# Kernel optimization log

Measured on AMD Instinct MI355X. Metric: run time of the kernel, lower is better.

Reference implementation:

```python
import jax, jax.numpy as jnp
import numpy as np

BATCH, SEQ, E, H = 8, 2048, 1024, 1024
LEAK = 0.95
SPECTRAL_RADIUS = 1.2
SPARSITY = 0.1


def setup_inputs() -> dict:
    rng = np.random.default_rng(0)
    x = rng.standard_normal((BATCH, SEQ, E)).astype(np.float32)
    # W_in: kaiming_uniform-like init
    bound = np.sqrt(1.0 / E)
    W_in = rng.uniform(-bound, bound, (H, E)).astype(np.float32)
    # W_res: sparse normal, rescaled to spectral radius 1.2
    W_res = rng.standard_normal((H, H)).astype(np.float32)
    mask = (rng.random((H, H)) > SPARSITY).astype(np.float32)
    W_res *= mask
    rad = np.max(np.abs(np.linalg.eigvals(W_res.astype(np.float64))))
    W_res = (W_res * (SPECTRAL_RADIUS / (rad + 1e-8))).astype(np.float32)
    s = 0.02
    inp = {
        "x": jnp.asarray(x),
        "W_in": jnp.asarray(W_in),
        "W_res": jnp.asarray(W_res),
        "norm_g": jnp.ones((E,), jnp.float32),
        "norm_b": jnp.zeros((E,), jnp.float32),
        "delta_w": jnp.asarray(rng.standard_normal((1, E)).astype(np.float32) * s),
        "delta_b": jnp.zeros((1,), jnp.float32),
        "A": jnp.full((H,), -10.0, jnp.float32),
        "B_w": jnp.asarray(rng.standard_normal((H, E)).astype(np.float32) * s),
        "ro_g": jnp.ones((H,), jnp.float32),
        "ro_b": jnp.zeros((H,), jnp.float32),
        "ro_w": jnp.asarray(rng.standard_normal((E, H)).astype(np.float32) * s),
        "ro_bias": jnp.zeros((E,), jnp.float32),
        "gate_w": jnp.asarray(rng.standard_normal((E, E)).astype(np.float32) * s),
        "gate_b": jnp.zeros((E,), jnp.float32),
    }
    return inp


def _layernorm(x, g, b, eps=1e-5):
    m = jnp.mean(x, axis=-1, keepdims=True)
    v = jnp.mean((x - m) ** 2, axis=-1, keepdims=True)
    return (x - m) * jax.lax.rsqrt(v + eps) * g + b


def reference(x, W_in, W_res, norm_g, norm_b, delta_w, delta_b, A, B_w,
              ro_g, ro_b, ro_w, ro_bias, gate_w, gate_b):
    x_norm = _layernorm(x, norm_g, norm_b)                      # [B,S,E]

    # --- TrueReservoir: leaky tanh RNN (scan over seq) ---
    xin = jnp.einsum('bse,he->bsh', x_norm, W_in)               # [B,S,H]
    h0 = jnp.zeros((x.shape[0], W_res.shape[0]), x.dtype)

    def res_step(h, u):
        new = jnp.tanh(u + h @ W_res.T)
        new = LEAK * new + (1.0 - LEAK) * h
        return new, new

    _, res_states = jax.lax.scan(res_step, h0, jnp.swapaxes(xin, 0, 1))
    res_states = jnp.swapaxes(res_states, 0, 1)                 # [B,S,H]

    ro_in = _layernorm(res_states, ro_g, ro_b)
    reservoir_out = jax.nn.gelu(jnp.einsum('bsh,eh->bse', ro_in, ro_w) + ro_bias,
                                approximate=False)              # [B,S,E]

    # --- selective SSM-style scan ---
    Bx = jnp.einsum('bse,he->bsh', x_norm, B_w)                 # [B,S,H]
    delta = jax.nn.softplus(jnp.einsum('bse,oe->bso', x_norm, delta_w) + delta_b)  # [B,S,1]
    A_bar = jnp.exp(A * delta)                                  # [B,S,H]
    B_bar = Bx * (1.0 - A_bar) / (A + 1e-8)                     # [B,S,H]

    def ssm_step(h, ab):
        a, b = ab
        h = a * h + b
        return h, h

    _, ssm_states = jax.lax.scan(
        ssm_step, h0, (jnp.swapaxes(A_bar, 0, 1), jnp.swapaxes(B_bar, 0, 1)))
    ssm_states = jnp.swapaxes(ssm_states, 0, 1)                 # [B,S,H]

    gate = jax.nn.sigmoid(jnp.einsum('bse,fe->bsf', x, gate_w) + gate_b)  # [B,S,E]
    return reservoir_out * gate + ssm_states * (1.0 - gate)
```

## Files before the change

### kernel.cpp

```cpp
#include <hip/hip_runtime.h>
#include <math.h>

#define B_ 8
#define S_ 2048
#define E_ 1024
#define H_ 1024
#define M_ 16384

typedef __attribute__((ext_vector_type(8))) short short8;
typedef __attribute__((ext_vector_type(4))) float floatx4;

__device__ __forceinline__ void block_reduce2(float &a, float &b) {
#pragma unroll
  for (int off = 32; off > 0; off >>= 1) {
    a += __shfl_down(a, off);
    b += __shfl_down(b, off);
  }
  __shared__ float sa[4], sb[4];
  const int w = threadIdx.x >> 6;
  __syncthreads();
  if ((threadIdx.x & 63) == 0) { sa[w] = a; sb[w] = b; }
  __syncthreads();
  a = sa[0] + sa[1] + sa[2] + sa[3];
  b = sb[0] + sb[1] + sb[2] + sb[3];
}

__device__ __forceinline__ unsigned pack_bf16(float lo, float hi) {
  return __builtin_amdgcn_perm(__float_as_uint(hi) + 0x8000u,
                               __float_as_uint(lo) + 0x8000u, 0x07060302u);
}
__device__ __forceinline__ unsigned pack_hi16(unsigned a, unsigned b) {
  return __builtin_amdgcn_perm(b, a, 0x07060302u);
}

__global__ __launch_bounds__(256) void ln_delta_kernel(
    const float* __restrict__ x, const float* __restrict__ g, const float* __restrict__ bt,
    const float* __restrict__ dw, const float* __restrict__ db,
    unsigned short* __restrict__ xnb, float* __restrict__ delta)
{
  const int row = blockIdx.x;
  const int t = threadIdx.x;
  const float4 v = ((const float4*)(x + (size_t)row * E_))[t];
  float s1 = v.x + v.y + v.z + v.w;
  float s2 = v.x*v.x + v.y*v.y + v.z*v.z + v.w*v.w;
  block_reduce2(s1, s2);
  const float mean = s1 * (1.f / E_);
  const float var  = s2 * (1.f / E_) - mean * mean;
  const float rstd = rsqrtf(var + 1e-5f);
  const float4 g4 = ((const float4*)g)[t];
  const float4 b4 = ((const float4*)bt)[t];
  float4 o;
  o.x = (v.x - mean) * rstd * g4.x + b4.x;
  o.y = (v.y - mean) * rstd * g4.y + b4.y;
  o.z = (v.z - mean) * rstd * g4.z + b4.z;
  o.w = (v.w - mean) * rstd * g4.w + b4.w;
  uint2 p;
  p.x = pack_bf16(o.x, o.y); p.y = pack_bf16(o.z, o.w);
  ((uint2*)(xnb + (size_t)row * E_))[t] = p;
  const float4 d4 = ((const float4*)dw)[t];
  float dd = o.x*d4.x + o.y*d4.y + o.z*d4.z + o.w*d4.w;
  float dummy = 0.f;
  block_reduce2(dd, dummy);
  if (t == 0) {
    const float z = dd + db[0];
    delta[row] = (z > 20.f) ? z : log1pf(__expf(z));
  }
}

__global__ __launch_bounds__(256) void rowstats_kernel(
    const float* __restrict__ res, float2* __restrict__ st)
{
  const int row = blockIdx.x;
  const int t = threadIdx.x;
  const float4 v = ((const float4*)(res + (size_t)row * H_))[t];
  float s1 = v.x + v.y + v.z + v.w;
  float s2 = v.x*v.x + v.y*v.y + v.z*v.z + v.w*v.w;
  block_reduce2(s1, s2);
  if (t == 0) {
    const float m = s1 * (1.f / H_);
    const float var = s2 * (1.f / H_) - m * m;
    st[row] = make_float2(m, rsqrtf(var + 1e-5f));
  }
}

__global__ __launch_bounds__(256) void tobf16_kernel(
    const float* __restrict__ s, unsigned short* __restrict__ d)
{
  const int i = blockIdx.x * 256 + threadIdx.x;
  const float4 v = ((const float4*)s)[i];
  uint2 p;
  p.x = pack_bf16(v.x, v.y); p.y = pack_bf16(v.z, v.w);
  ((uint2*)d)[i] = p;
}

__global__ __launch_bounds__(256) void splitw_kernel(
    const float* __restrict__ s, unsigned short* __restrict__ dh, unsigned short* __restrict__ dl)
{
  const int i = blockIdx.x * 256 + threadIdx.x;
  const float4 v = ((const float4*)s)[i];
  const float sv[4] = {v.x, v.y, v.z, v.w};
  unsigned h[4]; float l[4];
#pragma unroll
  for (int e = 0; e < 4; ++e) {
    h[e] = (__float_as_uint(sv[e]) + 0x8000u) & 0xFFFF0000u;
    l[e] = sv[e] - __uint_as_float(h[e]);
  }
  uint2 ph, pl;
  ph.x = pack_hi16(h[0], h[1]); ph.y = pack_hi16(h[2], h[3]);
  pl.x = pack_bf16(l[0], l[1]); pl.y = pack_bf16(l[2], l[3]);
  ((uint2*)dh)[i] = ph;
  ((uint2*)dl)[i] = pl;
}

__global__ __launch_bounds__(256) void gemm_bb(
    const unsigned short* __restrict__ A, const unsigned short* __restrict__ W,
    float* __restrict__ C)
{
  __shared__ __align__(16) unsigned short As[128 * 40];
  __shared__ __align__(16) unsigned short Ws[128 * 40];
  const int tid  = threadIdx.x;
  const int bn   = blockIdx.x & 7;
  const int bm   = blockIdx.x >> 3;
  const int wave = tid >> 6, lane = tid & 63;
  const int wm = (wave >> 1) * 64, wn = (wave & 1) * 64;
  const int fm = lane & 15, quad = lane >> 4;

  floatx4 acc[4][4];
#pragma unroll
  for (int i = 0; i < 4; ++i)
#pragma unroll
    for (int j = 0; j < 4; ++j) acc[i][j] = (floatx4){0.f, 0.f, 0.f, 0.f};

  const unsigned short* Abase = A + (size_t)bm * 128 * 1024;
  const unsigned short* Wbase = W + (size_t)bn * 128 * 1024;

  for (int k0 = 0; k0 < 1024; k0 += 32) {
    uint2 a2[4], w2[4];
#pragma unroll
    for (int i = 0; i < 4; ++i) {
      const int q = tid + 256 * i;
      const int row = q >> 3, ch = q & 7;
      a2[i] = *(const uint2*)(Abase + (size_t)row * 1024 + k0 + ch * 4);
      w2[i] = *(const uint2*)(Wbase + (size_t)row * 1024 + k0 + ch * 4);
    }
#pragma unroll
    for (int i = 0; i < 4; ++i) {
      const int q = tid + 256 * i;
      const int row = q >> 3, ch = q & 7;
      *(uint2*)(&As[row * 40 + ch * 4]) = a2[i];
      *(uint2*)(&Ws[row * 40 + ch * 4]) = w2[i];
    }
    __syncthreads();
    short8 af[4], wf[4];
#pragma unroll
    for (int i = 0; i < 4; ++i) {
      af[i] = *(const short8*)(&As[(wm + i * 16 + fm) * 40 + quad * 8]);
      wf[i] = *(const short8*)(&Ws[(wn + i * 16 + fm) * 40 + quad * 8]);
    }
#pragma unroll
    for (int i = 0; i < 4; ++i)
#pragma unroll
      for (int j = 0; j < 4; ++j)
        acc[i][j] = __builtin_amdgcn_mfma_f32_16x16x32_bf16(af[i], wf[j], acc[i][j], 0, 0, 0);
    __syncthreads();
  }

#pragma unroll
  for (int i = 0; i < 4; ++i) {
    const int grow0 = bm * 128 + wm + i * 16 + quad * 4;
#pragma unroll
    for (int j = 0; j < 4; ++j) {
      const int gcol = bn * 128 + wn + j * 16 + fm;
#pragma unroll
      for (int r = 0; r < 4; ++r)
        C[(size_t)(grow0 + r) * 1024 + gcol] = acc[i][j][r];
    }
  }
}

__global__ __launch_bounds__(256) void gemm_readout_mfma(
    const float* __restrict__ A,
    const unsigned short* __restrict__ Wh_g,
    const unsigned short* __restrict__ Wl_g,
    const float* __restrict__ bias,
    const float2* __restrict__ lnst,
    const float* __restrict__ lng, const float* __restrict__ lnb,
    const float* __restrict__ Avec,
    const float* __restrict__ cumd,
    const float* __restrict__ chH,
    const float* __restrict__ gate,
    float* __restrict__ C)
{
  __shared__ __align__(16) unsigned short Ah[128 * 40];
  __shared__ __align__(16) unsigned short Al[128 * 40];
  __shared__ __align__(16) unsigned short Wh[128 * 40];
  __shared__ __align__(16) unsigned short Wl[128 * 40];
  const int tid  = threadIdx.x;
  const int bn   = blockIdx.x & 7;
  const int bm   = blockIdx.x >> 3;
  const int wave = tid >> 6, lane = tid & 63;
  const int wm = (wave >> 1) * 64, wn = (wave & 1) * 64;
  const int fm = lane & 15, quad = lane >> 4;

  floatx4 acc[4][4];
#pragma unroll
  for (int i = 0; i < 4; ++i)
#pragma unroll
    for (int j = 0; j < 4; ++j) acc[i][j] = (floatx4){0.f, 0.f, 0.f, 0.f};

  const float* Abase = A + (size_t)bm * 128 * 1024;
  const unsigned short* Whb = Wh_g + (size_t)bn * 128 * 1024;
  const unsigned short* Wlb = Wl_g + (size_t)bn * 128 * 1024;

  float2 st_i[4];
#pragma unroll
  for (int i = 0; i < 4; ++i) {
    const int q = tid + 256 * i;
    st_i[i] = lnst[bm * 128 + (q >> 3)];
  }

  for (int k0 = 0; k0 < 1024; k0 += 32) {
#pragma unroll
    for (int i = 0; i < 4; ++i) {
      const int q = tid + 256 * i;
      const int row = q >> 3, ch = q & 7;
      float4 a4 = *(const float4*)(Abase + (size_t)row * 1024 + k0 + ch * 4);
      const float4 g4 = *(const float4*)(lng + k0 + ch * 4);
      const float4 b4 = *(const float4*)(lnb + k0 + ch * 4);
      const float2 st = st_i[i];
      a4.x = (a4.x - st.x) * st.y * g4.x + b4.x;
      a4.y = (a4.y - st.x) * st.y * g4.y + b4.y;
      a4.z = (a4.z - st.x) * st.y * g4.z + b4.z;
      a4.w = (a4.w - st.x) * st.y * g4.w + b4.w;
      const float av[4] = {a4.x, a4.y, a4.z, a4.w};
      unsigned ah[4]; float alr[4];
#pragma unroll
      for (int e = 0; e < 4; ++e) {
        ah[e] = (__float_as_uint(av[e]) + 0x8000u) & 0xFFFF0000u;
        alr[e] = av[e] - __uint_as_float(ah[e]);
      }
      uint2 pah, pal;
      pah.x = pack_hi16(ah[0], ah[1]); pah.y = pack_hi16(ah[2], ah[3]);
      pal.x = pack_bf16(alr[0], alr[1]); pal.y = pack_bf16(alr[2], alr[3]);
      *(uint2*)(&Ah[row * 40 + ch * 4]) = pah;
      *(uint2*)(&Al[row * 40 + ch * 4]) = pal;
      *(uint2*)(&Wh[row * 40 + ch * 4]) = *(const uint2*)(Whb + (size_t)row * 1024 + k0 + ch * 4);
      *(uint2*)(&Wl[row * 40 + ch * 4]) = *(const uint2*)(Wlb + (size_t)row * 1024 + k0 + ch * 4);
    }
    __syncthreads();
    short8 afh[4], afl[4], wfh[4], wfl[4];
#pragma unroll
    for (int i = 0; i < 4; ++i) {
      const int ao = (wm + i * 16 + fm) * 40 + quad * 8;
      const int wo = (wn + i * 16 + fm) * 40 + quad * 8;
      afh[i] = *(const short8*)(&Ah[ao]);
      afl[i] = *(const short8*)(&Al[ao]);
      wfh[i] = *(const short8*)(&Wh[wo]);
      wfl[i] = *(const short8*)(&Wl[wo]);
    }
#pragma unroll
    for (int i = 0; i < 4; ++i)
#pragma unroll
      for (int j = 0; j < 4; ++j) {
        acc[i][j] = __builtin_amdgcn_mfma_f32_16x16x32_bf16(afh[i], wfh[j], acc[i][j], 0, 0, 0);
        acc[i][j] = __builtin_amdgcn_mfma_f32_16x16x32_bf16(afl[i], wfh[j], acc[i][j], 0, 0, 0);
        acc[i][j] = __builtin_amdgcn_mfma_f32_16x16x32_bf16(afh[i], wfl[j], acc[i][j], 0, 0, 0);
      }
    __syncthreads();
  }

#pragma unroll
  for (int i = 0; i < 4; ++i) {
    const int grow0 = bm * 128 + wm + i * 16 + quad * 4;
    float cd_r[4];
    int hb_r[4];
#pragma unroll
    for (int r = 0; r < 4; ++r) {
      const int gr = grow0 + r;
      const int b = gr >> 11;
      const int c = (gr & 2047) >> 7;
      cd_r[r] = cumd[gr];
      hb_r[r] = (b * 16 + c) << 10;
    }
#pragma unroll
    for (int j = 0; j < 4; ++j) {
      const int gcol = bn * 128 + wn + j * 16 + fm;
      const float Ae = Avec[gcol];
      const float bb = bias[gcol];
#pragma unroll
      for (int r = 0; r < 4; ++r) {
        const int gr = grow0 + r;
        const size_t off = (size_t)gr * 1024 + gcol;
        const float hin = chH[hb_r[r] + gcol];
        const float lcl = C[off];
        const float gt  = gate[off];
        float v = acc[i][j][r] + bb;
        v = 0.5f * v * (1.f + erff(v * 0.70710678118654752f));
        const float p = __expf(Ae * cd_r[r]);
        const float sst = lcl + p * hin;
        C[off] = v * gt + sst * (1.f - gt);
      }
    }
  }
}

__global__ __launch_bounds__(512, 2) void scan_gate_kernel(
    float* __restrict__ xin_res,
    const float* __restrict__ Wres,
    unsigned* __restrict__ hbuf,
    const float* __restrict__ x,
    const float* __restrict__ gate_w,
    const float* __restrict__ gate_b,
    float* __restrict__ gateout,
    const float* __restrict__ delta,
    const float* __restrict__ Avec,
    float* __restrict__ bx,
    float* __restrict__ chP,
    float* __restrict__ cumd)
{
  __shared__ __align__(16) unsigned char smem[20480];
  const int wg  = blockIdx.x;
  const int tid = threadIdx.x;

  if (wg < 128) {
    float* hsb = (float*)smem;
    const int go  = wg & 7;
    const int mem = wg >> 3;
    const int g   = tid >> 6;
    const int l   = tid & 63;
    const int row8 = mem * 64 + g * 8;

    float4 w4[8][4];
#pragma unroll
    for (int r = 0; r < 8; ++r) {
      const float* wrow = Wres + (size_t)(row8 + r) * 1024 + l * 16;
#pragma unroll
      for (int j = 0; j < 4; ++j) w4[r][j] = *(const float4*)(wrow + 4 * j);
    }

    const int m0 = l & 1, m1 = (l >> 1) & 1, m2 = (l >> 2) & 1;
    const int myrow = row8 + (l & 7);
    float hprev = 0.f;
    const unsigned long long tmask = 0x0000FFFF0000FFFFull;

    const int Pw = (tid >> 1) ^ ((tid >> 6) & 7);
    const int wofs = Pw * 4 + (tid & 1) * 2;

    for (int s = 0; s < S_; ++s) {
      const float u = xin_res[((size_t)go * S_ + s) * H_ + myrow];
      asm volatile("" :: "v"(u));

      const unsigned tag = (unsigned)s & 0xFFFFu;
      const unsigned long long tag2 = (unsigned long long)tag | ((unsigned long long)tag << 32);
      const unsigned long long* hp =
          (const unsigned long long*)(hbuf + (size_t)(s & 1) * 8192 + go * 1024) + tid;
      unsigned long long w;
      for (;;) {
        w = __hip_atomic_load(hp, __ATOMIC_RELAXED, __HIP_MEMORY_SCOPE_AGENT);
        if (((w ^ tag2) & tmask) == 0ull) break;
      }

      float2 hf;
      hf.x = __uint_as_float((unsigned)w & 0xFFFF0000u);
      hf.y = __uint_as_float((unsigned)(w >> 32) & 0xFFFF0000u);
      *(float2*)(hsb + (s & 1) * 1024 + wofs) = hf;
      __syncthreads();

      const float* hbse = hsb + (s & 1) * 1024;
      float acc0 = 0.f, acc1 = 0.f, acc2 = 0.f, acc3 = 0.f;
      float acc4 = 0.f, acc5 = 0.f, acc6 = 0.f, acc7 = 0.f;
#pragma unroll
      for (int j = 0; j < 4; ++j) {
        const int P = (4 * l + j) ^ ((l >> 3) & 7);
        const float4 h4 = *(const float4*)(hbse + P * 4);
        acc0 += w4[0][j].x * h4.x + w4[0][j].y * h4.y + w4[0][j].z * h4.z + w4[0][j].w * h4.w;
        acc1 += w4[1][j].x * h4.x + w4[1][j].y * h4.y + w4[1][j].z * h4.z + w4[1][j].w * h4.w;
        acc2 += w4[2][j].x * h4.x + w4[2][j].y * h4.y + w4[2][j].z * h4.z + w4[2][j].w * h4.w;
        acc3 += w4[3][j].x * h4.x + w4[3][j].y * h4.y + w4[3][j].z * h4.z + w4[3][j].w * h4.w;
        acc4 += w4[4][j].x * h4.x + w4[4][j].y * h4.y + w4[4][j].z * h4.z + w4[4][j].w * h4.w;
        acc5 += w4[5][j].x * h4.x + w4[5][j].y * h4.y + w4[5][j].z * h4.z + w4[5][j].w * h4.w;
        acc6 += w4[6][j].x * h4.x + w4[6][j].y * h4.y + w4[6][j].z * h4.z + w4[6][j].w * h4.w;
        acc7 += w4[7][j].x * h4.x + w4[7][j].y * h4.y + w4[7][j].z * h4.z + w4[7][j].w * h4.w;
      }

      float v0 = (m0 ? acc1 : acc0) + __shfl_xor(m0 ? acc0 : acc1, 1);
      float v1 = (m0 ? acc3 : acc2) + __shfl_xor(m0 ? acc2 : acc3, 1);
      float v2 = (m0 ? acc5 : acc4) + __shfl_xor(m0 ? acc4 : acc5, 1);
      float v3 = (m0 ? acc7 : acc6) + __shfl_xor(m0 ? acc6 : acc7, 1);
      float u0 = (m1 ? v1 : v0) + __shfl_xor(m1 ? v0 : v1, 2);
      float u1 = (m1 ? v3 : v2) + __shfl_xor(m1 ? v2 : v3, 2);
      float ps = (m2 ? u1 : u0) + __shfl_xor(m2 ? u0 : u1, 4);
      ps += __shfl_xor(ps, 8);
      ps += __shfl_xor(ps, 16);
      ps += __shfl_xor(ps, 32);

      const float z  = u + ps;
      const float e  = __expf(2.f * z);
      const float hn = 1.f - __fdividef(2.f, e + 1.f);
      const float hv = 0.95f * hn + 0.05f * hprev;
      hprev = hv;

      if (l < 8) {
        const unsigned word = ((__float_as_uint(hv) + 0x8000u) & 0xFFFF0000u)
                            | ((unsigned)(s + 1) & 0xFFFFu);
        __hip_atomic_store(hbuf + (size_t)((s + 1) & 1) * 8192 + go * 1024 + myrow, word,
                           __ATOMIC_RELAXED, __HIP_MEMORY_SCOPE_AGENT);
        xin_res[((size_t)go * S_ + s) * H_ + myrow] = hv;
      }
    }
  } else if (wg < 1152) {
    unsigned short* As = (unsigned short*)smem;
    unsigned short* Ws = As + 128 * 40;
    const int bidx = wg - 128;
    const int bn   = bidx & 7;
    const int bm   = bidx >> 3;
    const bool act = tid < 256;
    const int wave = tid >> 6, lane = tid & 63;
    const int wm = (wave >> 1) * 64, wn = (wave & 1) * 64;
    const int fm = lane & 15, quad = lane >> 4;

    floatx4 acc[4][4];
#pragma unroll
    for (int i = 0; i < 4; ++i)
#pragma unroll
      for (int j = 0; j < 4; ++j) acc[i][j] = (floatx4){0.f, 0.f, 0.f, 0.f};

    const float* Abase = x + (size_t)bm * 128 * 1024;
    const float* Wbase = gate_w + (size_t)bn * 128 * 1024;

    for (int k0 = 0; k0 < 1024; k0 += 32) {
      if (act) {
        float4 a4[4], w4g[4];
#pragma unroll
        for (int i = 0; i < 4; ++i) {
          const int q = tid + 256 * i;
          const int row = q >> 3, ch = q & 7;
          a4[i]  = *(const float4*)(Abase + (size_t)row * 1024 + k0 + ch * 4);
          w4g[i] = *(const float4*)(Wbase + (size_t)row * 1024 + k0 + ch * 4);
        }
#pragma unroll
        for (int i = 0; i < 4; ++i) {
          const int q = tid + 256 * i;
          const int row = q >> 3, ch = q & 7;
          uint2 pa, pw;
          pa.x = pack_bf16(a4[i].x, a4[i].y);  pa.y = pack_bf16(a4[i].z, a4[i].w);
          pw.x = pack_bf16(w4g[i].x, w4g[i].y); pw.y = pack_bf16(w4g[i].z, w4g[i].w);
          *(uint2*)(&As[row * 40 + ch * 4]) = pa;
          *(uint2*)(&Ws[row * 40 + ch * 4]) = pw;
        }
      }
      __syncthreads();
      if (act) {
        short8 af[4], wf[4];
#pragma unroll
        for (int i = 0; i < 4; ++i) {
          af[i] = *(const short8*)(&As[(wm + i * 16 + fm) * 40 + quad * 8]);
          wf[i] = *(const short8*)(&Ws[(wn + i * 16 + fm) * 40 + quad * 8]);
        }
#pragma unroll
        for (int i = 0; i < 4; ++i)
#pragma unroll
          for (int j = 0; j < 4; ++j)
            acc[i][j] = __builtin_amdgcn_mfma_f32_16x16x32_bf16(af[i], wf[j], acc[i][j], 0, 0, 0);
      }
      __syncthreads();
    }

    if (act) {
#pragma unroll
      for (int i = 0; i < 4; ++i) {
        const int grow0 = bm * 128 + wm + i * 16 + quad * 4;
#pragma unroll
        for (int j = 0; j < 4; ++j) {
          const int gcol = bn * 128 + wn + j * 16 + fm;
          const float bb = gate_b[gcol];
#pragma unroll
          for (int r = 0; r < 4; ++r) {
            float v = acc[i][j][r] + bb;
            v = 1.f / (1.f + __expf(-v));
            gateout[(size_t)(grow0 + r) * 1024 + gcol] = v;
          }
        }
      }
    }
  } else if (wg < 1408) {
    const int idx = (wg - 1152) * 512 + tid;
    const int h = idx & 1023;
    const int c = (idx >> 10) & 15;
    const int b = idx >> 14;
    const float Ah = Avec[h];
    const float inv = 1.f / (Ah + 1e-8f);
    const float* dp = delta + b * S_ + c * 128;
    float* xp = bx + ((size_t)(b * S_ + c * 128)) * H_ + h;
    float p = 1.f, hl = 0.f;
    for (int t = 0; t < 128; ++t) {
      const float a = __expf(Ah * dp[t]);
      const float bb2 = xp[(size_t)t * H_] * (1.f - a) * inv;
      hl = a * hl + bb2;
      p *= a;
      xp[(size_t)t * H_] = hl;
    }
    chP[(b * 16 + c) * 1024 + h] = p;
  } else {
    if (tid < 128) {
      const int b = tid >> 4, c = tid & 15;
      const int base = b * S_ + c * 128;
      float acc = 0.f;
      for (int i = 0; i < 128; ++i) { acc += delta[base + i]; cumd[base + i] = acc; }
    }
  }
}

__global__ __launch_bounds__(256) void ssm_combine_kernel(
    const float* __restrict__ P, const float* __restrict__ local, float* __restrict__ Hin)
{
  const int idx = blockIdx.x * 256 + threadIdx.x;
  const int h = idx & 1023;
  const int b = idx >> 10;
  float hh = 0.f;
#pragma unroll
  for (int c = 0; c < 16; ++c) {
    const int o = (b * 16 + c) * 1024 + h;
    Hin[o] = hh;
    hh = P[o] * hh + local[((size_t)(b * S_ + c * 128 + 127)) * H_ + h];
  }
}

extern "C" void kernel_launch(void* const* d_in, const int* in_sizes, int n_in,
                              void* d_out, int out_size, void* d_ws, size_t ws_size,
                              hipStream_t stream) {
  (void)in_sizes; (void)n_in; (void)out_size; (void)ws_size;
  const float* x      = (const float*)d_in[0];
  const float* W_in   = (const float*)d_in[1];
  const float* W_res  = (const float*)d_in[2];
  const float* norm_g = (const float*)d_in[3];
  const float* norm_b = (const float*)d_in[4];
  const float* dw     = (const float*)d_in[5];
  const float* db     = (const float*)d_in[6];
  const float* Avec   = (const float*)d_in[7];
  const float* B_w    = (const float*)d_in[8];
  const float* ro_g   = (const float*)d_in[9];
  const float* ro_b   = (const float*)d_in[10];
  const float* ro_w   = (const float*)d_in[11];
  const float* ro_bias= (const float*)d_in[12];
  const float* gate_w = (const float*)d_in[13];
  const float* gate_b = (const float*)d_in[14];
  float* out = (float*)d_out;
  float* ws  = (float*)d_ws;

  float*    buf0   = ws;
  float*    buf1   = ws + 16777216;
  float*    delta  = ws + 33554432;
  float*    cumd   = ws + 33570816;
  unsigned* hbuf   = (unsigned*)(ws + 33587200);
  float2*   stats  = (float2*)(ws + 33603712);
  float*    chP    = ws + 33636480;
  float*    chH    = ws + 33767552;
  unsigned short* xnb = (unsigned short*)buf0;
  unsigned short* wib = (unsigned short*)(ws + 33898624);
  unsigned short* bwb = (unsigned short*)(ws + 34422912);
  unsigned short* roh = (unsigned short*)(ws + 34947200);
  unsigned short* rol = (unsigned short*)(ws + 35471488);

  tobf16_kernel<<<1024, 256, 0, stream>>>(W_in, wib);
  tobf16_kernel<<<1024, 256, 0, stream>>>(B_w, bwb);
  splitw_kernel<<<1024, 256, 0, stream>>>(ro_w, roh, rol);
  ln_delta_kernel<<<M_, 256, 0, stream>>>(x, norm_g, norm_b, dw, db, xnb, delta);
  gemm_bb<<<1024, 256, 0, stream>>>(xnb, wib, buf1);
  gemm_bb<<<1024, 256, 0, stream>>>(xnb, bwb, out);
  hipMemsetAsync(hbuf, 0, 2 * 8192 * sizeof(unsigned), stream);
  scan_gate_kernel<<<1409, 512, 0, stream>>>(buf1, W_res, hbuf, x, gate_w, gate_b, buf0,
                                             delta, Avec, out, chP, cumd);
  ssm_combine_kernel<<<32, 256, 0, stream>>>(chP, out, chH);
  rowstats_kernel<<<M_, 256, 0, stream>>>(buf1, stats);
  gemm_readout_mfma<<<1024, 256, 0, stream>>>(buf1, roh, rol, ro_bias, stats, ro_g, ro_b,
                                              Avec, cumd, chH, buf0, out);
}
```

Before: 3.442 ms.

## Fuse weight conversions, dual GEMMs, SSM combine and row stats into fewer launches

New measurement: 3.571 ms. +3.7%, slower.

```diff
diff --git a/kernel.cpp b/kernel.cpp
--- a/kernel.cpp
+++ b/kernel.cpp
@@ -67,60 +67,51 @@
   }
 }
 
-__global__ __launch_bounds__(256) void rowstats_kernel(
-    const float* __restrict__ res, float2* __restrict__ st)
+__global__ __launch_bounds__(256) void convert_kernel(
+    const float* __restrict__ W_in, const float* __restrict__ B_w, const float* __restrict__ ro_w,
+    unsigned short* __restrict__ wib, unsigned short* __restrict__ bwb,
+    unsigned short* __restrict__ roh, unsigned short* __restrict__ rol)
 {
-  const int row = blockIdx.x;
-  const int t = threadIdx.x;
-  const float4 v = ((const float4*)(res + (size_t)row * H_))[t];
-  float s1 = v.x + v.y + v.z + v.w;
-  float s2 = v.x*v.x + v.y*v.y + v.z*v.z + v.w*v.w;
-  block_reduce2(s1, s2);
-  if (t == 0) {
-    const float m = s1 * (1.f / H_);
-    const float var = s2 * (1.f / H_) - m * m;
-    st[row] = make_float2(m, rsqrtf(var + 1e-5f));
-  }
-}
-
-__global__ __launch_bounds__(256) void tobf16_kernel(
-    const float* __restrict__ s, unsigned short* __restrict__ d)
-{
-  const int i = blockIdx.x * 256 + threadIdx.x;
-  const float4 v = ((const float4*)s)[i];
-  uint2 p;
-  p.x = pack_bf16(v.x, v.y); p.y = pack_bf16(v.z, v.w);
-  ((uint2*)d)[i] = p;
-}
-
-__global__ __launch_bounds__(256) void splitw_kernel(
-    const float* __restrict__ s, unsigned short* __restrict__ dh, unsigned short* __restrict__ dl)
-{
-  const int i = blockIdx.x * 256 + threadIdx.x;
-  const float4 v = ((const float4*)s)[i];
-  const float sv[4] = {v.x, v.y, v.z, v.w};
-  unsigned h[4]; float l[4];
-#pragma unroll
-  for (int e = 0; e < 4; ++e) {
-    h[e] = (__float_as_uint(sv[e]) + 0x8000u) & 0xFFFF0000u;
-    l[e] = sv[e] - __uint_as_float(h[e]);
-  }
-  uint2 ph, pl;
-  ph.x = pack_hi16(h[0], h[1]); ph.y = pack_hi16(h[2], h[3]);
-  pl.x = pack_bf16(l[0], l[1]); pl.y = pack_bf16(l[2], l[3]);
-  ((uint2*)dh)[i] = ph;
-  ((uint2*)dl)[i] = pl;
-}
-
-__global__ __launch_bounds__(256) void gemm_bb(
-    const unsigned short* __restrict__ A, const unsigned short* __restrict__ W,
-    float* __restrict__ C)
+  const int b = blockIdx.x;
+  const int i = (b & 1023) * 256 + threadIdx.x;
+  if (b < 1024) {
+    const float4 v = ((const float4*)W_in)[i];
+    uint2 p; p.x = pack_bf16(v.x, v.y); p.y = pack_bf16(v.z, v.w);
+    ((uint2*)wib)[i] = p;
+  } else if (b < 2048) {
+    const float4 v = ((const float4*)B_w)[i];
+    uint2 p; p.x = pack_bf16(v.x, v.y); p.y = pack_bf16(v.z, v.w);
+    ((uint2*)bwb)[i] = p;
+  } else {
+    const float4 v = ((const float4*)ro_w)[i];
+    const float sv[4] = {v.x, v.y, v.z, v.w};
+    unsigned h[4]; float l[4];
+#pragma unroll
+    for (int e = 0; e < 4; ++e) {
+      h[e] = (__float_as_uint(sv[e]) + 0x8000u) & 0xFFFF0000u;
+      l[e] = sv[e] - __uint_as_float(h[e]);
+    }
+    uint2 ph, pl;
+    ph.x = pack_hi16(h[0], h[1]); ph.y = pack_hi16(h[2], h[3]);
+    pl.x = pack_bf16(l[0], l[1]); pl.y = pack_bf16(l[2], l[3]);
+    ((uint2*)roh)[i] = ph;
+    ((uint2*)rol)[i] = pl;
+  }
+}
+
+__global__ __launch_bounds__(256) void gemm_bb2(
+    const unsigned short* __restrict__ A,
+    const unsigned short* __restrict__ W0, const unsigned short* __restrict__ W1,
+    float* __restrict__ C0, float* __restrict__ C1)
 {
   __shared__ __align__(16) unsigned short As[128 * 40];
   __shared__ __align__(16) unsigned short Ws[128 * 40];
   const int tid  = threadIdx.x;
-  const int bn   = blockIdx.x & 7;
-  const int bm   = blockIdx.x >> 3;
+  const int bidx = blockIdx.x & 1023;
+  const unsigned short* W = (blockIdx.x < 1024) ? W0 : W1;
+  float* C = (blockIdx.x < 1024) ? C0 : C1;
+  const int bn   = bidx & 7;
+  const int bm   = bidx >> 3;
   const int wave = tid >> 6, lane = tid & 63;
   const int wm = (wave >> 1) * 64, wn = (wave & 1) * 64;
   const int fm = lane & 15, quad = lane >> 4;
@@ -183,7 +174,6 @@
     const unsigned short* __restrict__ Wh_g,
     const unsigned short* __restrict__ Wl_g,
     const float* __restrict__ bias,
-    const float2* __restrict__ lnst,
     const float* __restrict__ lng, const float* __restrict__ lnb,
     const float* __restrict__ Avec,
     const float* __restrict__ cumd,
@@ -212,11 +202,28 @@
   const unsigned short* Whb = Wh_g + (size_t)bn * 128 * 1024;
   const unsigned short* Wlb = Wl_g + (size_t)bn * 128 * 1024;
 
+  float s1[4] = {0.f, 0.f, 0.f, 0.f}, s2[4] = {0.f, 0.f, 0.f, 0.f};
+  for (int k0 = 0; k0 < 1024; k0 += 32) {
+#pragma unroll
+    for (int i = 0; i < 4; ++i) {
+      const int q = tid + 256 * i;
+      const int row = q >> 3, ch = q & 7;
+      const float4 a4 = *(const float4*)(Abase + (size_t)row * 1024 + k0 + ch * 4);
+      s1[i] += a4.x + a4.y + a4.z + a4.w;
+      s2[i] += a4.x*a4.x + a4.y*a4.y + a4.z*a4.z + a4.w*a4.w;
+    }
+  }
   float2 st_i[4];
 #pragma unroll
   for (int i = 0; i < 4; ++i) {
-    const int q = tid + 256 * i;
-    st_i[i] = lnst[bm * 128 + (q >> 3)];
+#pragma unroll
+    for (int off = 1; off < 8; off <<= 1) {
+      s1[i] += __shfl_xor(s1[i], off);
+      s2[i] += __shfl_xor(s2[i], off);
+    }
+    const float m  = s1[i] * (1.f / 1024.f);
+    const float va = s2[i] * (1.f / 1024.f) - m * m;
+    st_i[i] = make_float2(m, rsqrtf(va + 1e-5f));
   }
 
   for (int k0 = 0; k0 < 1024; k0 += 32) {
@@ -316,7 +323,9 @@
     const float* __restrict__ Avec,
     float* __restrict__ bx,
     float* __restrict__ chP,
-    float* __restrict__ cumd)
+    float* __restrict__ cumd,
+    float* __restrict__ chH,
+    unsigned* __restrict__ ctr)
 {
   __shared__ __align__(16) unsigned char smem[20480];
   const int wg  = blockIdx.x;
@@ -501,28 +510,29 @@
       xp[(size_t)t * H_] = hl;
     }
     chP[(b * 16 + c) * 1024 + h] = p;
-  } else {
+    __syncthreads();
+    if (tid == 0)
+      __hip_atomic_fetch_add(ctr, 1u, __ATOMIC_RELEASE, __HIP_MEMORY_SCOPE_AGENT);
+  } else if (wg == 1408) {
     if (tid < 128) {
       const int b = tid >> 4, c = tid & 15;
       const int base = b * S_ + c * 128;
       float acc = 0.f;
       for (int i = 0; i < 128; ++i) { acc += delta[base + i]; cumd[base + i] = acc; }
     }
-  }
-}
-
-__global__ __launch_bounds__(256) void ssm_combine_kernel(
-    const float* __restrict__ P, const float* __restrict__ local, float* __restrict__ Hin)
-{
-  const int idx = blockIdx.x * 256 + threadIdx.x;
-  const int h = idx & 1023;
-  const int b = idx >> 10;
-  float hh = 0.f;
-#pragma unroll
-  for (int c = 0; c < 16; ++c) {
-    const int o = (b * 16 + c) * 1024 + h;
-    Hin[o] = hh;
-    hh = P[o] * hh + local[((size_t)(b * S_ + c * 128 + 127)) * H_ + h];
+  } else {
+    while (__hip_atomic_load(ctr, __ATOMIC_ACQUIRE, __HIP_MEMORY_SCOPE_AGENT) < 256u)
+      __builtin_amdgcn_s_sleep(8);
+    const int idx = (wg - 1409) * 512 + tid;
+    const int h = idx & 1023;
+    const int b = idx >> 10;
+    float hh = 0.f;
+#pragma unroll
+    for (int c = 0; c < 16; ++c) {
+      const int o = (b * 16 + c) * 1024 + h;
+      chH[o] = hh;
+      hh = chP[o] * hh + bx[((size_t)(b * S_ + c * 128 + 127)) * H_ + h];
+    }
   }
 }
 
@@ -553,7 +563,7 @@
   float*    delta  = ws + 33554432;
   float*    cumd   = ws + 33570816;
   unsigned* hbuf   = (unsigned*)(ws + 33587200);
-  float2*   stats  = (float2*)(ws + 33603712);
+  unsigned* ctr    = hbuf + 16384;
   float*    chP    = ws + 33636480;
   float*    chH    = ws + 33767552;
   unsigned short* xnb = (unsigned short*)buf0;
@@ -562,17 +572,12 @@
   unsigned short* roh = (unsigned short*)(ws + 34947200);
   unsigned short* rol = (unsigned short*)(ws + 35471488);
 
-  tobf16_kernel<<<1024, 256, 0, stream>>>(W_in, wib);
-  tobf16_kernel<<<1024, 256, 0, stream>>>(B_w, bwb);
-  splitw_kernel<<<1024, 256, 0, stream>>>(ro_w, roh, rol);
+  convert_kernel<<<3072, 256, 0, stream>>>(W_in, B_w, ro_w, wib, bwb, roh, rol);
   ln_delta_kernel<<<M_, 256, 0, stream>>>(x, norm_g, norm_b, dw, db, xnb, delta);
-  gemm_bb<<<1024, 256, 0, stream>>>(xnb, wib, buf1);
-  gemm_bb<<<1024, 256, 0, stream>>>(xnb, bwb, out);
-  hipMemsetAsync(hbuf, 0, 2 * 8192 * sizeof(unsigned), stream);
-  scan_gate_kernel<<<1409, 512, 0, stream>>>(buf1, W_res, hbuf, x, gate_w, gate_b, buf0,
-                                             delta, Avec, out, chP, cumd);
-  ssm_combine_kernel<<<32, 256, 0, stream>>>(chP, out, chH);
-  rowstats_kernel<<<M_, 256, 0, stream>>>(buf1, stats);
-  gemm_readout_mfma<<<1024, 256, 0, stream>>>(buf1, roh, rol, ro_bias, stats, ro_g, ro_b,
+  gemm_bb2<<<2048, 256, 0, stream>>>(xnb, wib, bwb, buf1, out);
+  hipMemsetAsync(hbuf, 0, 2 * 8192 * sizeof(unsigned) + 128, stream);
+  scan_gate_kernel<<<1425, 512, 0, stream>>>(buf1, W_res, hbuf, x, gate_w, gate_b, buf0,
+                                             delta, Avec, out, chP, cumd, chH, ctr);
+  gemm_readout_mfma<<<1024, 256, 0, stream>>>(buf1, roh, rol, ro_bias, ro_g, ro_b,
                                               Avec, cumd, chH, buf0, out);
 }
```
